# Optimization experiments

Hardware: AMD Instinct MI355X
Metric: run time of the kernel (lower is better)

## Reference

```python
import jax, jax.numpy as jnp
from jax import lax
import numpy as np

BETA = 6.6


def _conv(x, w, b=None, stride=1, pad=0):
    # x: NCHW, w: OIHW (torch layout)
    y = lax.conv_general_dilated(x, w, (stride, stride), [(pad, pad), (pad, pad)],
                                 dimension_numbers=('NCHW', 'OIHW', 'NCHW'))
    if b is not None:
        y = y + b[None, :, None, None]
    return y


def _conv_t(x, w, b, stride=2, pad=1):
    # torch ConvTranspose2d: w is [in, out, kH, kW]; equivalent to dilated conv with flipped kernel
    k = w.shape[2]
    w2 = jnp.flip(w, (2, 3)).transpose(1, 0, 2, 3)  # -> OIHW
    y = lax.conv_general_dilated(x, w2, (1, 1), [(k - 1 - pad, k - 1 - pad)] * 2,
                                 lhs_dilation=(stride, stride),
                                 dimension_numbers=('NCHW', 'OIHW', 'NCHW'))
    return y + b[None, :, None, None]


def _res_stack(x, pairs):
    for wa, wb in pairs:
        x = x + _conv(jax.nn.relu(_conv(jax.nn.relu(x), wa, pad=1)), wb, pad=1)
    return jax.nn.relu(x)


def _quantize(z, E, beta):
    # z: [B, D, H, W]; E: [K, D]
    xp = z.transpose(0, 2, 3, 1)                       # BHWD
    flat = xp.reshape(-1, E.shape[1])                  # [N, D]
    d = (jnp.sum(flat ** 2, axis=1, keepdims=True)
         + jnp.sum(E ** 2, axis=1)
         - 2.0 * flat @ E.T)                           # [N, K]
    idx = jnp.argmin(d, axis=1)                        # [N]
    q = E[idx].reshape(xp.shape)                       # gather == onehot @ E
    loss_q = jnp.mean((q - lax.stop_gradient(xp)) ** 2)
    loss_e = jnp.mean((lax.stop_gradient(q) - xp) ** 2)
    loss = loss_q + beta * loss_e
    q_st = xp + lax.stop_gradient(q - xp)              # straight-through
    z_q = q_st.transpose(0, 3, 1, 2)
    counts = jnp.zeros((E.shape[0],), jnp.float32).at[idx].add(1.0)
    probs = counts / flat.shape[0]
    perplexity = jnp.exp(-jnp.sum(probs * jnp.log(probs + 1e-10)))
    return loss, z_q, perplexity


def setup_inputs() -> dict:
    key = jax.random.key(0)
    ks = iter(jax.random.split(key, 32))

    def p(*s):
        return jax.random.normal(next(ks), s, jnp.float32) * 0.05

    inp = dict(
        x=jax.random.normal(next(ks), (32, 3, 256, 256), jnp.float32),
        # encoder
        w1=p(64, 3, 4, 4), b1=p(64),
        w2=p(128, 64, 4, 4), b2=p(128),
        w3=p(128, 128, 3, 3), b3=p(128),
        r0a=p(32, 128, 3, 3), r0b=p(128, 32, 3, 3),
        r1a=p(32, 128, 3, 3), r1b=p(128, 32, 3, 3),
        # pre-VQ 1x1 conv
        wp=p(64, 128, 1, 1), bp=p(64),
        # codebook
        E=jax.random.uniform(next(ks), (512, 64), jnp.float32, -1.0 / 512, 1.0 / 512),
        # decoder
        dw1=p(128, 64, 3, 3), db1=p(128),
        dr0a=p(32, 128, 3, 3), dr0b=p(128, 32, 3, 3),
        dr1a=p(32, 128, 3, 3), dr1b=p(128, 32, 3, 3),
        tw1=p(128, 64, 4, 4), tb1=p(64),   # ConvTranspose2d(128,64,4,2,1) torch layout [in,out,k,k]
        tw2=p(64, 3, 4, 4), tb2=p(3),      # ConvTranspose2d(64,3,4,2,1)
    )
    return inp


def reference(x, w1, b1, w2, b2, w3, b3, r0a, r0b, r1a, r1b, wp, bp, E,
              dw1, db1, dr0a, dr0b, dr1a, dr1b, tw1, tb1, tw2, tb2):
    # Encoder
    z = jax.nn.relu(_conv(x, w1, b1, stride=2, pad=1))
    z = jax.nn.relu(_conv(z, w2, b2, stride=2, pad=1))
    z = _conv(z, w3, b3, stride=1, pad=1)
    z = _res_stack(z, [(r0a, r0b), (r1a, r1b)])
    # pre-VQ projection
    z = _conv(z, wp, bp)
    # Vector quantization
    loss, z_q, perplexity = _quantize(z, E, BETA)
    # Decoder
    d = _conv(z_q, dw1, db1, pad=1)
    d = _res_stack(d, [(dr0a, dr0b), (dr1a, dr1b)])
    d = jax.nn.relu(_conv_t(d, tw1, tb1))
    x_tilda = _conv_t(d, tw2, tb2)
    return (loss, x_tilda, perplexity)
```

## Files before the change

### kernel.cpp

```cpp
#include <hip/hip_runtime.h>
#include <math.h>

typedef __attribute__((ext_vector_type(8))) short bf16x8;
typedef __attribute__((ext_vector_type(4))) float f32x4;

__device__ inline float bf2f(ushort u) {
    union { uint i; float f; } v; v.i = ((uint)u) << 16; return v.f;
}
__device__ inline ushort f2bf(float f) {
    union { float f; uint i; } v; v.f = f;
    uint b = v.i;
    b += 0x7FFFu + ((b >> 16) & 1u);
    return (ushort)(b >> 16);
}
__device__ inline uint relu2bf(uint x) {
    uint s = x & 0x80008000u;
    uint m = (s >> 15) * 0xFFFFu;
    return x & ~m;
}

template<int CIN, int COUT, int NT>
__global__ __launch_bounds__(256) void wt_oihw(const float* __restrict__ s, ushort* __restrict__ d) {
    int i = blockIdx.x * 256 + threadIdx.x;
    if (i >= COUT * NT * CIN) return;
    int co = i / (NT * CIN);
    int r  = i % (NT * CIN);
    int tap = r / CIN, ci = r % CIN;
    d[i] = f2bf(s[(co * CIN + ci) * NT + tap]);
}

__global__ __launch_bounds__(256) void wt_tconv1(const float* __restrict__ s, ushort* __restrict__ d) {
    int i = blockIdx.x * 256 + threadIdx.x;
    if (i >= 4 * 64 * 512) return;
    int cls = i >> 15;
    int co  = (i >> 9) & 63;
    int k   = i & 511;
    int tap = k >> 7, ci = k & 127;
    int a = tap >> 1, b = tap & 1;
    int ph = cls >> 1, pw = cls & 1;
    int kh = ph ? (a ? 2 : 0) : (a ? 3 : 1);
    int kw = pw ? (b ? 2 : 0) : (b ? 3 : 1);
    d[i] = f2bf(s[((ci * 64 + co) << 4) + kh * 4 + kw]);
}

__global__ __launch_bounds__(256) void vq_prep(const float* __restrict__ E,
                                               ushort* __restrict__ Ebf, float* __restrict__ eN) {
    int i = blockIdx.x * 256 + threadIdx.x;
    if (i < 32768) Ebf[i] = f2bf(E[i]);
    if (i < 512) {
        float s = 0.f;
        #pragma unroll 8
        for (int d = 0; d < 64; ++d) { float x = E[i * 64 + d]; s = fmaf(x, x, s); }
        eN[i] = s;
    }
}

template<int CIN, int COUT, int NT, int HALO, bool RELU_A, bool RELU_OUT, bool HAS_RES>
__global__ __launch_bounds__(256)
void conv_lds(const ushort* __restrict__ in, const ushort* __restrict__ wt,
              const float* __restrict__ bias, const ushort* __restrict__ res,
              ushort* __restrict__ out) {
    constexpr int K = NT * CIN;
    constexpr int KSTEPS = K / 32;
    constexpr int CSTEPS = CIN / 32;
    constexpr int PR = HALO ? 4 : 2;
    constexpr int PC = HALO ? 66 : 64;
    constexpr int CIP = CIN + 8;
    constexpr int WM = (COUT == 128) ? 4 : 2;
    constexpr int WN = (COUT == 32) ? 2 : 4;
    constexpr int NC8 = CIN / 8;
    constexpr int NLD = PR * PC * NC8;

    __shared__ ushort sP[PR * PC * CIP];

    const int t = threadIdx.x;
    const int w = t >> 6, l = t & 63;
    const int bid = blockIdx.x;
    const int n = bid >> 5, R = bid & 31;

    const int m0 = (COUT == 128) ? 64 * (w >> 1) : 32 * w;
    const int n0 = (COUT == 128) ? 64 * (w & 1) : 0;

    for (int i = t; i < NLD; i += 256) {
        const int c8  = i & (NC8 - 1);
        const int rem = i / NC8;
        const int pc  = rem % PC;
        const int pr  = rem / PC;
        const int grow = 2 * R - HALO + pr;
        const int gcol = pc - HALO;
        uint4 v = make_uint4(0u, 0u, 0u, 0u);
        if (!HALO || ((unsigned)grow < 64u && (unsigned)gcol < 64u))
            v = *reinterpret_cast<const uint4*>(
                in + (((long long)(n * 64 + grow)) * 64 + gcol) * CIN + c8 * 8);
        if (RELU_A) {
            v.x = relu2bf(v.x); v.y = relu2bf(v.y);
            v.z = relu2bf(v.z); v.w = relu2bf(v.w);
        }
        *reinterpret_cast<uint4*>(&sP[(pr * PC + pc) * CIP + c8 * 8]) = v;
    }
    __syncthreads();

    int aoff[WM];
    #pragma unroll
    for (int mf = 0; mf < WM; ++mf) {
        const int px = m0 + mf * 16 + (l & 15);
        aoff[mf] = ((px >> 6) * PC + (px & 63)) * CIP + ((l >> 4) * 8);
    }

    f32x4 acc[WM][WN] = {};

    for (int ks = 0; ks < KSTEPS; ++ks) {
        const int tap = (CSTEPS == 1) ? ks : ks / CSTEPS;
        const int ci0 = (CSTEPS == 1) ? 0 : (ks % CSTEPS) * 32;
        int dh = 0, dw = 0;
        if (NT == 9) { dh = tap / 3 - 1; dw = tap % 3 - 1; }
        const int base = ((dh + HALO) * PC + (dw + HALO)) * CIP + ci0;

        bf16x8 bfr[WN];
        #pragma unroll
        for (int nf = 0; nf < WN; ++nf)
            bfr[nf] = *reinterpret_cast<const bf16x8*>(
                wt + (n0 + nf * 16 + (l & 15)) * K + ks * 32 + ((l >> 4) * 8));

        #pragma unroll
        for (int mf = 0; mf < WM; ++mf) {
            bf16x8 afr = *reinterpret_cast<const bf16x8*>(&sP[base + aoff[mf]]);
            #pragma unroll
            for (int nf = 0; nf < WN; ++nf)
                acc[mf][nf] = __builtin_amdgcn_mfma_f32_16x16x32_bf16(
                    afr, bfr[nf], acc[mf][nf], 0, 0, 0);
        }
    }

    #pragma unroll
    for (int mf = 0; mf < WM; ++mf) {
        #pragma unroll
        for (int nf = 0; nf < WN; ++nf) {
            const int col = n0 + nf * 16 + (l & 15);
            const float bv = bias ? bias[col] : 0.f;
            #pragma unroll
            for (int r = 0; r < 4; ++r) {
                const int prow = m0 + mf * 16 + ((l >> 4) * 4) + r;
                const int orow = 2 * R + (prow >> 6);
                const int ocol = prow & 63;
                const long long oidx = (((long long)(n * 64 + orow)) * 64 + ocol) * COUT + col;
                float v = acc[mf][nf][r] + bv;
                if (HAS_RES) v += bf2f(res[oidx]);
                if (RELU_OUT) v = fmaxf(v, 0.f);
                out[oidx] = f2bf(v);
            }
        }
    }
}

__global__ __launch_bounds__(256)
void convt1_lds(const ushort* __restrict__ in, const ushort* __restrict__ wt,
                const float* __restrict__ bias, ushort* __restrict__ out) {
    constexpr int CIN = 128, CIP = 136, PC = 66;
    __shared__ ushort sP[4 * PC * CIP];

    const int t = threadIdx.x;
    const int w = t >> 6, l = t & 63;
    const int bid = blockIdx.x;
    const int n = bid >> 5, R = bid & 31;

    for (int i = t; i < 4 * PC * 16; i += 256) {
        const int c8  = i & 15;
        const int rem = i >> 4;
        const int pc  = rem % PC;
        const int pr  = rem / PC;
        const int grow = 2 * R - 1 + pr;
        const int gcol = pc - 1;
        uint4 v = make_uint4(0u, 0u, 0u, 0u);
        if ((unsigned)grow < 64u && (unsigned)gcol < 64u)
            v = *reinterpret_cast<const uint4*>(
                in + (((long long)(n * 64 + grow)) * 64 + gcol) * CIN + c8 * 8);
        *reinterpret_cast<uint4*>(&sP[(pr * PC + pc) * CIP + c8 * 8]) = v;
    }
    __syncthreads();

    const int ph = w >> 1, pw = w & 1;
    const ushort* wc = wt + w * 32768;

    int aoff[8];
    #pragma unroll
    for (int mf = 0; mf < 8; ++mf) {
        const int px = mf * 16 + (l & 15);
        aoff[mf] = ((px >> 6) * PC + (px & 63)) * CIP + ((l >> 4) * 8);
    }

    f32x4 acc[8][4] = {};

    for (int ks = 0; ks < 16; ++ks) {
        const int tap = ks >> 2, ci0 = (ks & 3) * 32;
        const int a = tap >> 1, b = tap & 1;
        const int dh = ph ? 1 - a : -a;
        const int dw = pw ? 1 - b : -b;
        const int base = ((dh + 1) * PC + (dw + 1)) * CIP + ci0;

        bf16x8 bfr[4];
        #pragma unroll
        for (int nf = 0; nf < 4; ++nf)
            bfr[nf] = *reinterpret_cast<const bf16x8*>(
                wc + (nf * 16 + (l & 15)) * 512 + ks * 32 + ((l >> 4) * 8));

        #pragma unroll
        for (int mf = 0; mf < 8; ++mf) {
            bf16x8 afr = *reinterpret_cast<const bf16x8*>(&sP[base + aoff[mf]]);
            #pragma unroll
            for (int nf = 0; nf < 4; ++nf)
                acc[mf][nf] = __builtin_amdgcn_mfma_f32_16x16x32_bf16(
                    afr, bfr[nf], acc[mf][nf], 0, 0, 0);
        }
    }

    #pragma unroll
    for (int mf = 0; mf < 8; ++mf) {
        #pragma unroll
        for (int nf = 0; nf < 4; ++nf) {
            const int col = nf * 16 + (l & 15);
            const float bv = bias[col];
            #pragma unroll
            for (int r = 0; r < 4; ++r) {
                const int prow = mf * 16 + ((l >> 4) * 4) + r;
                const int orow = 2 * R + (prow >> 6);
                const int ocol = prow & 63;
                const long long oidx =
                    (((long long)(n * 128 + 2 * orow + ph)) * 128 + 2 * ocol + pw) * 64 + col;
                float v = fmaxf(acc[mf][nf][r] + bv, 0.f);
                out[oidx] = f2bf(v);
            }
        }
    }
}

template<int CIN, int COUT, bool RELU_OUT>
__global__ __launch_bounds__(256)
void conv_s2(const ushort* __restrict__ in, const ushort* __restrict__ wt,
             const float* __restrict__ bias, ushort* __restrict__ out,
             int Hin, int Win) {
    constexpr int K = 16 * CIN;
    constexpr int KSTEPS = K / 32;
    constexpr int CSTEPS = CIN / 32;
    constexpr int WM = 4, WN = 4;

    __shared__ ushort sA[2][128 * 40];

    const int t = threadIdx.x;
    const int w = t >> 6, l = t & 63;
    const int bid = blockIdx.x;
    const int n = bid >> 5, R = bid & 31;

    const int m0 = 64 * (w >> 1);
    const int n0 = 64 * (w & 1);

    const int gpx  = t >> 1;
    const int gk   = (t & 1) * 16;
    const int grow = 2 * R + (gpx >> 6);
    const int gcol = gpx & 63;

    auto gather = [&](int ks, uint4& g0, uint4& g1) {
        int tap, ci0;
        if (CSTEPS == 1) { tap = ks; ci0 = 0; }
        else             { tap = ks / CSTEPS; ci0 = (ks % CSTEPS) * 32; }
        const int dh = tap / 4 - 1, dw = tap % 4 - 1;
        const int ih = 2 * grow + dh, iw = 2 * gcol + dw;
        g0 = make_uint4(0u, 0u, 0u, 0u); g1 = g0;
        if ((unsigned)ih < (unsigned)Hin && (unsigned)iw < (unsigned)Win) {
            const ushort* p = in + (((long long)(n * Hin + ih)) * Win + iw) * CIN + ci0 + gk;
            g0 = *reinterpret_cast<const uint4*>(p);
            g1 = *reinterpret_cast<const uint4*>(p + 8);
        }
    };

    f32x4 acc[WM][WN] = {};

    uint4 g0, g1;
    gather(0, g0, g1);
    *reinterpret_cast<uint4*>(&sA[0][gpx * 40 + gk])     = g0;
    *reinterpret_cast<uint4*>(&sA[0][gpx * 40 + gk + 8]) = g1;
    __syncthreads();

    int cur = 0;
    for (int ks = 0; ks < KSTEPS; ++ks) {
        const bool more = (ks + 1 < KSTEPS);
        uint4 h0, h1;
        if (more) gather(ks + 1, h0, h1);

        bf16x8 bfr[WN];
        #pragma unroll
        for (int nf = 0; nf < WN; ++nf)
            bfr[nf] = *reinterpret_cast<const bf16x8*>(
                wt + (n0 + nf * 16 + (l & 15)) * K + ks * 32 + ((l >> 4) * 8));

        bf16x8 afr[WM];
        #pragma unroll
        for (int mf = 0; mf < WM; ++mf)
            afr[mf] = *reinterpret_cast<const bf16x8*>(
                &sA[cur][(m0 + mf * 16 + (l & 15)) * 40 + ((l >> 4) * 8)]);

        #pragma unroll
        for (int mf = 0; mf < WM; ++mf)
            #pragma unroll
            for (int nf = 0; nf < WN; ++nf)
                acc[mf][nf] = __builtin_amdgcn_mfma_f32_16x16x32_bf16(
                    afr[mf], bfr[nf], acc[mf][nf], 0, 0, 0);

        if (more) {
            *reinterpret_cast<uint4*>(&sA[cur ^ 1][gpx * 40 + gk])     = h0;
            *reinterpret_cast<uint4*>(&sA[cur ^ 1][gpx * 40 + gk + 8]) = h1;
            __syncthreads();
            cur ^= 1;
        }
    }

    #pragma unroll
    for (int mf = 0; mf < WM; ++mf) {
        #pragma unroll
        for (int nf = 0; nf < WN; ++nf) {
            const int col = n0 + nf * 16 + (l & 15);
            const float bv = bias[col];
            #pragma unroll
            for (int r = 0; r < 4; ++r) {
                const int prow = m0 + mf * 16 + ((l >> 4) * 4) + r;
                const int orow = 2 * R + (prow >> 6);
                const int ocol = prow & 63;
                const long long oidx = (((long long)(n * 64 + orow)) * 64 + ocol) * COUT + col;
                float v = acc[mf][nf][r] + bv;
                if (RELU_OUT) v = fmaxf(v, 0.f);
                out[oidx] = f2bf(v);
            }
        }
    }
}

__global__ __launch_bounds__(256)
void conv1_k(const float* __restrict__ x, const float* __restrict__ w1,
             const float* __restrict__ b1, ushort* __restrict__ out) {
    __shared__ float sIn[3 * 4 * 36];
    __shared__ float sW[64 * 49];
    const int t = threadIdx.x;
    const int bid = blockIdx.x;
    const int n = bid >> 7, oh = bid & 127;
    const int ow0 = blockIdx.y * 16;

    for (int i = t; i < 3072; i += 256) {
        int co = i / 48, k = i % 48;
        sW[co * 49 + k] = w1[i];
    }
    for (int i = t; i < 3 * 4 * 34; i += 256) {
        int ci = i / 136, r = i - ci * 136;
        int r4 = r / 34, iwl = r % 34;
        int ih = 2 * oh - 1 + r4;
        int iw = 2 * ow0 - 1 + iwl;
        float v = 0.f;
        if ((unsigned)ih < 256u && (unsigned)iw < 256u)
            v = x[((n * 3 + ci) * 256 + ih) * 256 + iw];
        sIn[ci * 144 + r4 * 36 + iwl] = v;
    }
    __syncthreads();

    const int co = t & 63, j = t >> 6;
    float wr[48];
    #pragma unroll
    for (int i = 0; i < 48; ++i) wr[i] = sW[co * 49 + i];
    const float bv = b1[co];

    #pragma unroll
    for (int q = 0; q < 4; ++q) {
        const int owl = j * 4 + q;
        float acc = bv;
        #pragma unroll
        for (int ci = 0; ci < 3; ++ci)
            #pragma unroll
            for (int kh = 0; kh < 4; ++kh)
                #pragma unroll
                for (int kw = 0; kw < 4; ++kw)
                    acc = fmaf(sIn[ci * 144 + kh * 36 + 2 * owl + kw],
                               wr[ci * 16 + kh * 4 + kw], acc);
        acc = fmaxf(acc, 0.f);
        out[(((long long)(n * 128 + oh)) * 128 + ow0 + owl) * 64 + co] = f2bf(acc);
    }
}

__global__ __launch_bounds__(256)
void convt2_k(const ushort* __restrict__ in, const float* __restrict__ tw2,
              const float* __restrict__ tb2, float* __restrict__ out) {
    __shared__ float sW[64 * 48];
    const int t = threadIdx.x;
    for (int i = t; i < 3072; i += 256) sW[i] = tw2[i];
    __syncthreads();

    const int bid = blockIdx.x;
    const int n = bid >> 8, oh = bid & 255;
    const int ow = t;
    const int khA = (oh + 1) & 1, ihA = (oh + 1) >> 1;
    const int kwA = (ow + 1) & 1, iwA = (ow + 1) >> 1;

    float a0 = tb2[0], a1 = tb2[1], a2 = tb2[2];
    #pragma unroll
    for (int a = 0; a < 2; ++a) {
        const int ih = ihA - a;
        if ((unsigned)ih >= 128u) continue;
        const int kh = khA + 2 * a;
        #pragma unroll
        for (int b = 0; b < 2; ++b) {
            const int iw = iwA - b;
            if ((unsigned)iw >= 128u) continue;
            const int kw = kwA + 2 * b;
            const ushort* src = in + (((long long)(n * 128 + ih)) * 128 + iw) * 64;
            const int k = kh * 4 + kw;
            #pragma unroll
            for (int c8 = 0; c8 < 8; ++c8) {
                uint4 v = *reinterpret_cast<const uint4*>(src + c8 * 8);
                const uint u[4] = {v.x, v.y, v.z, v.w};
                #pragma unroll
                for (int p = 0; p < 4; ++p) {
                    union { uint i; float f; } lo, hi;
                    lo.i = u[p] << 16; hi.i = u[p] & 0xFFFF0000u;
                    const int ci = c8 * 8 + p * 2;
                    a0 = fmaf(lo.f, sW[ci * 48 + 0 * 16 + k], a0);
                    a1 = fmaf(lo.f, sW[ci * 48 + 1 * 16 + k], a1);
                    a2 = fmaf(lo.f, sW[ci * 48 + 2 * 16 + k], a2);
                    a0 = fmaf(hi.f, sW[(ci + 1) * 48 + 0 * 16 + k], a0);
                    a1 = fmaf(hi.f, sW[(ci + 1) * 48 + 1 * 16 + k], a1);
                    a2 = fmaf(hi.f, sW[(ci + 1) * 48 + 2 * 16 + k], a2);
                }
            }
        }
    }
    const long long px = (long long)oh * 256 + ow;
    out[(long long)(n * 3 + 0) * 65536 + px] = a0;
    out[(long long)(n * 3 + 1) * 65536 + px] = a1;
    out[(long long)(n * 3 + 2) * 65536 + px] = a2;
}

__global__ __launch_bounds__(256)
void vq_mfma(const ushort* __restrict__ z, const ushort* __restrict__ Ebf,
             const float* __restrict__ E, const float* __restrict__ eN,
             ushort* __restrict__ zq, float* __restrict__ stats) {
    __shared__ ushort sZ[64 * 72];
    __shared__ float sEN[512];
    __shared__ float sV[64 * 4];
    __shared__ int   sI[64 * 4];
    __shared__ int   sIdx[64];
    __shared__ unsigned shist[512];
    __shared__ float red[256];

    const int t = threadIdx.x;
    const int w = t >> 6, l = t & 63;
    const long long p0 = (long long)blockIdx.x * 64;

    {
        const int px = t >> 2, koff = (t & 3) * 16;
        const ushort* p = z + (p0 + px) * 64 + koff;
        uint4 a0 = *reinterpret_cast<const uint4*>(p);
        uint4 a1 = *reinterpret_cast<const uint4*>(p + 8);
        *reinterpret_cast<uint4*>(&sZ[px * 72 + koff])     = a0;
        *reinterpret_cast<uint4*>(&sZ[px * 72 + koff + 8]) = a1;
        sEN[t] = eN[t]; sEN[t + 256] = eN[t + 256];
        shist[t] = 0u; shist[t + 256] = 0u;
    }
    __syncthreads();

    f32x4 acc[4][8] = {};
    #pragma unroll
    for (int ks = 0; ks < 2; ++ks) {
        bf16x8 bfr[8];
        #pragma unroll
        for (int nf = 0; nf < 8; ++nf)
            bfr[nf] = *reinterpret_cast<const bf16x8*>(
                Ebf + (w * 128 + nf * 16 + (l & 15)) * 64 + ks * 32 + ((l >> 4) * 8));
        #pragma unroll
        for (int mf = 0; mf < 4; ++mf) {
            bf16x8 afr = *reinterpret_cast<const bf16x8*>(
                &sZ[(mf * 16 + (l & 15)) * 72 + ks * 32 + ((l >> 4) * 8)]);
            #pragma unroll
            for (int nf = 0; nf < 8; ++nf)
                acc[mf][nf] = __builtin_amdgcn_mfma_f32_16x16x32_bf16(
                    afr, bfr[nf], acc[mf][nf], 0, 0, 0);
        }
    }

    float eNr[8];
    #pragma unroll
    for (int nf = 0; nf < 8; ++nf) eNr[nf] = sEN[w * 128 + nf * 16 + (l & 15)];

    #pragma unroll
    for (int mf = 0; mf < 4; ++mf) {
        #pragma unroll
        for (int r = 0; r < 4; ++r) {
            float best = 3.4e38f; int bidx = 0;
            #pragma unroll
            for (int nf = 0; nf < 8; ++nf) {
                float s = eNr[nf] - 2.f * acc[mf][nf][r];
                int   c = w * 128 + nf * 16 + (l & 15);
                if (s < best || (s == best && c < bidx)) { best = s; bidx = c; }
            }
            #pragma unroll
            for (int off = 1; off < 16; off <<= 1) {
                float ov = __shfl_xor(best, off);
                int   oi = __shfl_xor(bidx, off);
                if (ov < best || (ov == best && oi < bidx)) { best = ov; bidx = oi; }
            }
            if ((l & 15) == 0) {
                const int px = mf * 16 + ((l >> 4) * 4) + r;
                sV[px * 4 + w] = best; sI[px * 4 + w] = bidx;
            }
        }
    }
    __syncthreads();

    if (t < 64) {
        float best = sV[t * 4]; int bidx = sI[t * 4];
        #pragma unroll
        for (int w2 = 1; w2 < 4; ++w2) {
            float v = sV[t * 4 + w2]; int c = sI[t * 4 + w2];
            if (v < best || (v == best && c < bidx)) { best = v; bidx = c; }
        }
        sIdx[t] = bidx;
        atomicAdd(&shist[bidx], 1u);
    }
    __syncthreads();

    {
        const int px = t >> 2, doff = (t & 3) * 16;
        const int idx = sIdx[px];
        const float* e = E + idx * 64 + doff;
        float dist = 0.f;
        uint4 pk4[2];
        ushort* pk = reinterpret_cast<ushort*>(pk4);
        #pragma unroll
        for (int j = 0; j < 16; ++j) {
            float ev = e[j];
            float zv = bf2f(sZ[px * 72 + doff + j]);
            float df = ev - zv;
            dist = fmaf(df, df, dist);
            pk[j] = f2bf(ev);
        }
        *reinterpret_cast<uint4*>(zq + (p0 + px) * 64 + doff)     = pk4[0];
        *reinterpret_cast<uint4*>(zq + (p0 + px) * 64 + doff + 8) = pk4[1];
        red[t] = dist;
    }
    __syncthreads();
    for (int s = 128; s > 0; s >>= 1) {
        if (t < s) red[t] += red[t + s];
        __syncthreads();
    }
    if (t == 0) atomicAdd(&stats[0], red[0]);
    for (int i = t; i < 512; i += 256) {
        unsigned c = shist[i];
        if (c) atomicAdd(&stats[1 + i], (float)c);
    }
}

__global__ __launch_bounds__(512)
void finalize_kernel(const float* __restrict__ stats, float* __restrict__ out, int plast) {
    __shared__ float red[512];
    int t = threadIdx.x;
    float c = stats[1 + t];
    float p = c * (1.f / 131072.f);
    red[t] = p * logf(p + 1e-10f);
    __syncthreads();
    for (int s = 256; s > 0; s >>= 1) {
        if (t < s) red[t] += red[t + s];
        __syncthreads();
    }
    if (t == 0) {
        out[plast] = expf(-red[0]);
        out[0] = 7.6f * stats[0] * (1.f / 8388608.f);
    }
}

extern "C" void kernel_launch(void* const* d_in, const int* in_sizes, int n_in,
                              void* d_out, int out_size, void* d_ws, size_t ws_size,
                              hipStream_t stream) {
    (void)in_sizes; (void)n_in; (void)ws_size;
    const float* x   = (const float*)d_in[0];
    const float* w1  = (const float*)d_in[1];
    const float* b1  = (const float*)d_in[2];
    const float* w2  = (const float*)d_in[3];
    const float* b2  = (const float*)d_in[4];
    const float* w3  = (const float*)d_in[5];
    const float* b3  = (const float*)d_in[6];
    const float* r0a = (const float*)d_in[7];
    const float* r0b = (const float*)d_in[8];
    const float* r1a = (const float*)d_in[9];
    const float* r1b = (const float*)d_in[10];
    const float* wp  = (const float*)d_in[11];
    const float* bp  = (const float*)d_in[12];
    const float* E   = (const float*)d_in[13];
    const float* dw1 = (const float*)d_in[14];
    const float* db1 = (const float*)d_in[15];
    const float* dr0a= (const float*)d_in[16];
    const float* dr0b= (const float*)d_in[17];
    const float* dr1a= (const float*)d_in[18];
    const float* dr1b= (const float*)d_in[19];
    const float* tw1 = (const float*)d_in[20];
    const float* tb1 = (const float*)d_in[21];
    const float* tw2 = (const float*)d_in[22];
    const float* tb2 = (const float*)d_in[23];

    float* out = (float*)d_out;
    ushort* ws = (ushort*)d_ws;

    ushort* H1 = ws;
    ushort* H2 = ws + 33554432;
    ushort* C  = ws + 50331648;
    ushort* F  = ws + 67108864;
    ushort* Z  = ws + 71303168;
    ushort* ZQ = ws + 79691776;
    ushort* W0 = ws + 88080384;
    ushort* Wt2   = W0;
    ushort* Wt3   = W0 + 131072;
    ushort* Wr0a  = W0 + 278528;
    ushort* Wr0b  = W0 + 315392;
    ushort* Wr1a  = W0 + 352256;
    ushort* Wr1b  = W0 + 389120;
    ushort* Wp    = W0 + 425984;
    ushort* Wd1   = W0 + 434176;
    ushort* Wdr0a = W0 + 507904;
    ushort* Wdr0b = W0 + 544768;
    ushort* Wdr1a = W0 + 581632;
    ushort* Wdr1b = W0 + 618496;
    ushort* WT1   = W0 + 655360;
    ushort* Ebf   = W0 + 786432;
    float*  eN    = (float*)(W0 + 819200);
    float*  ST    = (float*)(W0 + 820224);
    ushort* T = H1;
    ushort* D = H2;

    hipMemsetAsync(ST, 0, 513 * sizeof(float), stream);

    dim3 blk(256);
    wt_oihw<64, 128,16><<<512, blk, 0, stream>>>(w2,  Wt2);
    wt_oihw<128,128, 9><<<576, blk, 0, stream>>>(w3,  Wt3);
    wt_oihw<128, 32, 9><<<144, blk, 0, stream>>>(r0a, Wr0a);
    wt_oihw<32, 128, 9><<<144, blk, 0, stream>>>(r0b, Wr0b);
    wt_oihw<128, 32, 9><<<144, blk, 0, stream>>>(r1a, Wr1a);
    wt_oihw<32, 128, 9><<<144, blk, 0, stream>>>(r1b, Wr1b);
    wt_oihw<128, 64, 1><<<32,  blk, 0, stream>>>(wp,  Wp);
    wt_oihw<64, 128, 9><<<288, blk, 0, stream>>>(dw1, Wd1);
    wt_oihw<128, 32, 9><<<144, blk, 0, stream>>>(dr0a, Wdr0a);
    wt_oihw<32, 128, 9><<<144, blk, 0, stream>>>(dr0b, Wdr0b);
    wt_oihw<128, 32, 9><<<144, blk, 0, stream>>>(dr1a, Wdr1a);
    wt_oihw<32, 128, 9><<<144, blk, 0, stream>>>(dr1b, Wdr1b);
    wt_tconv1<<<512, blk, 0, stream>>>(tw1, WT1);
    vq_prep<<<128, blk, 0, stream>>>(E, Ebf, eN);

    conv1_k<<<dim3(32 * 128, 8), blk, 0, stream>>>(x, w1, b1, H1);
    conv_s2<64,128,true><<<1024, blk, 0, stream>>>(H1, Wt2, b2, H2, 128, 128);
    conv_lds<128,128,9,1,false,false,false><<<1024, blk, 0, stream>>>(H2, Wt3, b3, nullptr, C);
    conv_lds<128, 32,9,1,true ,true ,false><<<1024, blk, 0, stream>>>(C, Wr0a, nullptr, nullptr, F);
    conv_lds<32, 128,9,1,false,false,true ><<<1024, blk, 0, stream>>>(F, Wr0b, nullptr, C, C);
    conv_lds<128, 32,9,1,true ,true ,false><<<1024, blk, 0, stream>>>(C, Wr1a, nullptr, nullptr, F);
    conv_lds<32, 128,9,1,false,true ,true ><<<1024, blk, 0, stream>>>(F, Wr1b, nullptr, C, C);
    conv_lds<128, 64,1,0,false,false,false><<<1024, blk, 0, stream>>>(C, Wp, bp, nullptr, Z);

    vq_mfma<<<2048, blk, 0, stream>>>(Z, Ebf, E, eN, ZQ, ST);

    conv_lds<64, 128,9,1,false,false,false><<<1024, blk, 0, stream>>>(ZQ, Wd1, db1, nullptr, D);
    conv_lds<128, 32,9,1,true ,true ,false><<<1024, blk, 0, stream>>>(D, Wdr0a, nullptr, nullptr, F);
    conv_lds<32, 128,9,1,false,false,true ><<<1024, blk, 0, stream>>>(F, Wdr0b, nullptr, D, D);
    conv_lds<128, 32,9,1,true ,true ,false><<<1024, blk, 0, stream>>>(D, Wdr1a, nullptr, nullptr, F);
    conv_lds<32, 128,9,1,false,true ,true ><<<1024, blk, 0, stream>>>(F, Wdr1b, nullptr, D, D);
    convt1_lds<<<1024, blk, 0, stream>>>(D, WT1, tb1, T);
    convt2_k<<<32 * 256, blk, 0, stream>>>(T, tw2, tb2, out + 1);

    finalize_kernel<<<1, 512, 0, stream>>>(ST, out, out_size - 1);
}
```

Measured before the change: 1.232 ms.

## Run first conv as bf16 MFMA GEMM and merge weight-prep kernels

The first encoder conv (3->64, 4x4, stride 2) moves from scalar fp32 FMAs to an im2col tile in LDS followed by bf16 MFMA 16x16x32, with K padded from 48 to 64. Each block now covers a full output row of 128 pixels. The fourteen separate weight-conversion and codebook-prep launches are merged into one kernel, which also converts w1 to padded bf16, cutting launch overhead. In exchange the conv1 inputs are rounded to bf16, which adds precision error.

```diff
diff --git a/kernel.cpp b/kernel.cpp
--- a/kernel.cpp
+++ b/kernel.cpp
@@ -20,8 +20,7 @@
 }
 
 template<int CIN, int COUT, int NT>
-__global__ __launch_bounds__(256) void wt_oihw(const float* __restrict__ s, ushort* __restrict__ d) {
-    int i = blockIdx.x * 256 + threadIdx.x;
+__device__ inline void wt_body(int i, const float* __restrict__ s, ushort* __restrict__ d) {
     if (i >= COUT * NT * CIN) return;
     int co = i / (NT * CIN);
     int r  = i % (NT * CIN);
@@ -29,29 +28,133 @@
     d[i] = f2bf(s[(co * CIN + ci) * NT + tap]);
 }
 
-__global__ __launch_bounds__(256) void wt_tconv1(const float* __restrict__ s, ushort* __restrict__ d) {
-    int i = blockIdx.x * 256 + threadIdx.x;
-    if (i >= 4 * 64 * 512) return;
-    int cls = i >> 15;
-    int co  = (i >> 9) & 63;
-    int k   = i & 511;
-    int tap = k >> 7, ci = k & 127;
-    int a = tap >> 1, b = tap & 1;
-    int ph = cls >> 1, pw = cls & 1;
-    int kh = ph ? (a ? 2 : 0) : (a ? 3 : 1);
-    int kw = pw ? (b ? 2 : 0) : (b ? 3 : 1);
-    d[i] = f2bf(s[((ci * 64 + co) << 4) + kh * 4 + kw]);
-}
-
-__global__ __launch_bounds__(256) void vq_prep(const float* __restrict__ E,
-                                               ushort* __restrict__ Ebf, float* __restrict__ eN) {
-    int i = blockIdx.x * 256 + threadIdx.x;
-    if (i < 32768) Ebf[i] = f2bf(E[i]);
-    if (i < 512) {
-        float s = 0.f;
-        #pragma unroll 8
-        for (int d = 0; d < 64; ++d) { float x = E[i * 64 + d]; s = fmaf(x, x, s); }
-        eN[i] = s;
+__global__ __launch_bounds__(256)
+void wt_all(const float* w2, ushort* Wt2, const float* w3, ushort* Wt3,
+            const float* r0a, ushort* Wr0a, const float* r0b, ushort* Wr0b,
+            const float* r1a, ushort* Wr1a, const float* r1b, ushort* Wr1b,
+            const float* wp,  ushort* Wp,   const float* dw1, ushort* Wd1,
+            const float* dr0a, ushort* Wdr0a, const float* dr0b, ushort* Wdr0b,
+            const float* dr1a, ushort* Wdr1a, const float* dr1b, ushort* Wdr1b,
+            const float* tw1, ushort* WT1,
+            const float* E, ushort* Ebf, float* eN,
+            const float* w1, ushort* Wc1) {
+    const int b = blockIdx.x, t = threadIdx.x;
+    if (b < 512)        { wt_body<64, 128,16>(b * 256 + t, w2,  Wt2); }
+    else if (b < 1088)  { wt_body<128,128, 9>((b-512) * 256 + t, w3, Wt3); }
+    else if (b < 1232)  { wt_body<128, 32, 9>((b-1088) * 256 + t, r0a, Wr0a); }
+    else if (b < 1376)  { wt_body<32, 128, 9>((b-1232) * 256 + t, r0b, Wr0b); }
+    else if (b < 1520)  { wt_body<128, 32, 9>((b-1376) * 256 + t, r1a, Wr1a); }
+    else if (b < 1664)  { wt_body<32, 128, 9>((b-1520) * 256 + t, r1b, Wr1b); }
+    else if (b < 1696)  { wt_body<128, 64, 1>((b-1664) * 256 + t, wp,  Wp); }
+    else if (b < 1984)  { wt_body<64, 128, 9>((b-1696) * 256 + t, dw1, Wd1); }
+    else if (b < 2128)  { wt_body<128, 32, 9>((b-1984) * 256 + t, dr0a, Wdr0a); }
+    else if (b < 2272)  { wt_body<32, 128, 9>((b-2128) * 256 + t, dr0b, Wdr0b); }
+    else if (b < 2416)  { wt_body<128, 32, 9>((b-2272) * 256 + t, dr1a, Wdr1a); }
+    else if (b < 2560)  { wt_body<32, 128, 9>((b-2416) * 256 + t, dr1b, Wdr1b); }
+    else if (b < 3072) {
+        int i = (b - 2560) * 256 + t;
+        if (i < 4 * 64 * 512) {
+            int cls = i >> 15;
+            int co  = (i >> 9) & 63;
+            int k   = i & 511;
+            int tap = k >> 7, ci = k & 127;
+            int a = tap >> 1, bb = tap & 1;
+            int ph = cls >> 1, pw = cls & 1;
+            int kh = ph ? (a ? 2 : 0) : (a ? 3 : 1);
+            int kw = pw ? (bb ? 2 : 0) : (bb ? 3 : 1);
+            WT1[i] = f2bf(tw1[((ci * 64 + co) << 4) + kh * 4 + kw]);
+        }
+    } else if (b < 3200) {
+        int i = (b - 3072) * 256 + t;
+        if (i < 32768) Ebf[i] = f2bf(E[i]);
+        if (i < 512) {
+            float s = 0.f;
+            #pragma unroll 8
+            for (int d = 0; d < 64; ++d) { float xx = E[i * 64 + d]; s = fmaf(xx, xx, s); }
+            eN[i] = s;
+        }
+    } else {
+        int i = (b - 3200) * 256 + t;
+        if (i < 4096) {
+            int co = i >> 6, k = i & 63;
+            Wc1[i] = (k < 48) ? f2bf(w1[co * 48 + k]) : (ushort)0;
+        }
+    }
+}
+
+__global__ __launch_bounds__(256)
+void conv1_mfma(const float* __restrict__ x, const ushort* __restrict__ wt,
+                const float* __restrict__ b1, ushort* __restrict__ out) {
+    __shared__ float  sIn[3 * 4 * 264];
+    __shared__ ushort sA[128 * 72];
+
+    const int t = threadIdx.x;
+    const int w = t >> 6, l = t & 63;
+    const int bid = blockIdx.x;
+    const int n = bid >> 7, oh = bid & 127;
+
+    for (int i = t; i < 3 * 4 * 258; i += 256) {
+        const int ci = i / 1032, rem = i % 1032;
+        const int r4 = rem / 258, c = rem % 258;
+        const int ih = 2 * oh - 1 + r4, iw = c - 1;
+        float v = 0.f;
+        if ((unsigned)ih < 256u && (unsigned)iw < 256u)
+            v = x[((n * 3 + ci) * 256 + ih) * 256 + iw];
+        sIn[(ci * 4 + r4) * 264 + c] = v;
+    }
+    __syncthreads();
+
+    for (int i = t; i < 128 * 6; i += 256) {
+        const int px = i / 6, seg = i % 6, k0 = seg * 8;
+        ushort pk[8];
+        #pragma unroll
+        for (int j = 0; j < 8; ++j) {
+            const int k = k0 + j;
+            float v = 0.f;
+            if (k < 48) {
+                const int ci = k >> 4, kh = (k >> 2) & 3, kw = k & 3;
+                v = sIn[(ci * 4 + kh) * 264 + 2 * px + kw];
+            }
+            pk[j] = f2bf(v);
+        }
+        *reinterpret_cast<uint4*>(&sA[px * 72 + k0]) =
+            *reinterpret_cast<const uint4*>(pk);
+    }
+    __syncthreads();
+
+    const int m0 = 32 * w;
+    f32x4 acc[2][4] = {};
+    #pragma unroll
+    for (int ks = 0; ks < 2; ++ks) {
+        bf16x8 bfr[4];
+        #pragma unroll
+        for (int nf = 0; nf < 4; ++nf)
+            bfr[nf] = *reinterpret_cast<const bf16x8*>(
+                wt + (nf * 16 + (l & 15)) * 64 + ks * 32 + ((l >> 4) * 8));
+        #pragma unroll
+        for (int mf = 0; mf < 2; ++mf) {
+            bf16x8 afr = *reinterpret_cast<const bf16x8*>(
+                &sA[(m0 + mf * 16 + (l & 15)) * 72 + ks * 32 + ((l >> 4) * 8)]);
+            #pragma unroll
+            for (int nf = 0; nf < 4; ++nf)
+                acc[mf][nf] = __builtin_amdgcn_mfma_f32_16x16x32_bf16(
+                    afr, bfr[nf], acc[mf][nf], 0, 0, 0);
+        }
+    }
+
+    #pragma unroll
+    for (int mf = 0; mf < 2; ++mf) {
+        #pragma unroll
+        for (int nf = 0; nf < 4; ++nf) {
+            const int col = nf * 16 + (l & 15);
+            const float bv = b1[col];
+            #pragma unroll
+            for (int r = 0; r < 4; ++r) {
+                const int ow = m0 + mf * 16 + ((l >> 4) * 4) + r;
+                float v = fmaxf(acc[mf][nf][r] + bv, 0.f);
+                out[(((long long)(n * 128 + oh)) * 128 + ow) * 64 + col] = f2bf(v);
+            }
+        }
     }
 }
 
@@ -331,55 +434,6 @@
                 out[oidx] = f2bf(v);
             }
         }
-    }
-}
-
-__global__ __launch_bounds__(256)
-void conv1_k(const float* __restrict__ x, const float* __restrict__ w1,
-             const float* __restrict__ b1, ushort* __restrict__ out) {
-    __shared__ float sIn[3 * 4 * 36];
-    __shared__ float sW[64 * 49];
-    const int t = threadIdx.x;
-    const int bid = blockIdx.x;
-    const int n = bid >> 7, oh = bid & 127;
-    const int ow0 = blockIdx.y * 16;
-
-    for (int i = t; i < 3072; i += 256) {
-        int co = i / 48, k = i % 48;
-        sW[co * 49 + k] = w1[i];
-    }
-    for (int i = t; i < 3 * 4 * 34; i += 256) {
-        int ci = i / 136, r = i - ci * 136;
-        int r4 = r / 34, iwl = r % 34;
-        int ih = 2 * oh - 1 + r4;
-        int iw = 2 * ow0 - 1 + iwl;
-        float v = 0.f;
-        if ((unsigned)ih < 256u && (unsigned)iw < 256u)
-            v = x[((n * 3 + ci) * 256 + ih) * 256 + iw];
-        sIn[ci * 144 + r4 * 36 + iwl] = v;
-    }
-    __syncthreads();
-
-    const int co = t & 63, j = t >> 6;
-    float wr[48];
-    #pragma unroll
-    for (int i = 0; i < 48; ++i) wr[i] = sW[co * 49 + i];
-    const float bv = b1[co];
-
-    #pragma unroll
-    for (int q = 0; q < 4; ++q) {
-        const int owl = j * 4 + q;
-        float acc = bv;
-        #pragma unroll
-        for (int ci = 0; ci < 3; ++ci)
-            #pragma unroll
-            for (int kh = 0; kh < 4; ++kh)
-                #pragma unroll
-                for (int kw = 0; kw < 4; ++kw)
-                    acc = fmaf(sIn[ci * 144 + kh * 36 + 2 * owl + kw],
-                               wr[ci * 16 + kh * 4 + kw], acc);
-        acc = fmaxf(acc, 0.f);
-        out[(((long long)(n * 128 + oh)) * 128 + ow0 + owl) * 64 + co] = f2bf(acc);
     }
 }
 
@@ -627,28 +681,19 @@
     ushort* Ebf   = W0 + 786432;
     float*  eN    = (float*)(W0 + 819200);
     float*  ST    = (float*)(W0 + 820224);
+    ushort* Wc1   = W0 + 822272;
     ushort* T = H1;
     ushort* D = H2;
 
     hipMemsetAsync(ST, 0, 513 * sizeof(float), stream);
 
     dim3 blk(256);
-    wt_oihw<64, 128,16><<<512, blk, 0, stream>>>(w2,  Wt2);
-    wt_oihw<128,128, 9><<<576, blk, 0, stream>>>(w3,  Wt3);
-    wt_oihw<128, 32, 9><<<144, blk, 0, stream>>>(r0a, Wr0a);
-    wt_oihw<32, 128, 9><<<144, blk, 0, stream>>>(r0b, Wr0b);
-    wt_oihw<128, 32, 9><<<144, blk, 0, stream>>>(r1a, Wr1a);
-    wt_oihw<32, 128, 9><<<144, blk, 0, stream>>>(r1b, Wr1b);
-    wt_oihw<128, 64, 1><<<32,  blk, 0, stream>>>(wp,  Wp);
-    wt_oihw<64, 128, 9><<<288, blk, 0, stream>>>(dw1, Wd1);
-    wt_oihw<128, 32, 9><<<144, blk, 0, stream>>>(dr0a, Wdr0a);
-    wt_oihw<32, 128, 9><<<144, blk, 0, stream>>>(dr0b, Wdr0b);
-    wt_oihw<128, 32, 9><<<144, blk, 0, stream>>>(dr1a, Wdr1a);
-    wt_oihw<32, 128, 9><<<144, blk, 0, stream>>>(dr1b, Wdr1b);
-    wt_tconv1<<<512, blk, 0, stream>>>(tw1, WT1);
-    vq_prep<<<128, blk, 0, stream>>>(E, Ebf, eN);
-
-    conv1_k<<<dim3(32 * 128, 8), blk, 0, stream>>>(x, w1, b1, H1);
+    wt_all<<<3216, blk, 0, stream>>>(w2, Wt2, w3, Wt3, r0a, Wr0a, r0b, Wr0b,
+                                     r1a, Wr1a, r1b, Wr1b, wp, Wp, dw1, Wd1,
+                                     dr0a, Wdr0a, dr0b, Wdr0b, dr1a, Wdr1a, dr1b, Wdr1b,
+                                     tw1, WT1, E, Ebf, eN, w1, Wc1);
+
+    conv1_mfma<<<4096, blk, 0, stream>>>(x, Wc1, b1, H1);
     conv_s2<64,128,true><<<1024, blk, 0, stream>>>(H1, Wt2, b2, H2, 128, 128);
     conv_lds<128,128,9,1,false,false,false><<<1024, blk, 0, stream>>>(H2, Wt3, b3, nullptr, C);
     conv_lds<128, 32,9,1,true ,true ,false><<<1024, blk, 0, stream>>>(C, Wr0a, nullptr, nullptr, F);
```

Result: faster. 1.103 ms (-10.4%).
